# Kernel tuning notes

Hardware: AMD Instinct MI355X
Metric: run time of the kernel (lower is better)

## Reference

```python
import jax, jax.numpy as jnp
import numpy as np
import math

B, T, C, H, S = 2, 2048, 1024, 16, 16
HD = C // H
EPS = 1e-5


def setup_inputs() -> dict:
    key = jax.random.key(0)
    ks = jax.random.split(key, 20)
    sc = 1.0 / math.sqrt(C)
    inp = {
        "x": jax.random.normal(ks[0], (B, T, C), jnp.float32),
        # A_log_fwd: log(arange(1..S)) repeated over dim (as in __init__)
        "A_log": jnp.log(jnp.tile(jnp.arange(1, S + 1, dtype=jnp.float32), (C, 1))),
        # Linear weights stored (in, out); apply as x @ W + b
        "Wd": jax.random.normal(ks[1], (C, C), jnp.float32) * sc,
        "bd": jnp.full((C,), -3.0, jnp.float32),
        "WB": jax.random.normal(ks[2], (C, S), jnp.float32) * sc,
        "WC": jax.random.normal(ks[3], (C, S), jnp.float32) * sc,
        "Wq": jax.random.normal(ks[4], (C, C), jnp.float32) * sc,
        "bq": jnp.zeros((C,), jnp.float32),
        "Wk": jax.random.normal(ks[5], (C, C), jnp.float32) * sc,
        "bk": jnp.zeros((C,), jnp.float32),
        "Wv": jax.random.normal(ks[6], (C, C), jnp.float32) * sc,
        "bv": jnp.zeros((C,), jnp.float32),
        "Wx": jax.random.normal(ks[7], (C, C), jnp.float32) * sc,
        "bx": jnp.zeros((C,), jnp.float32),
        "Wo": jax.random.normal(ks[8], (C, C), jnp.float32) * sc,
        "bo": jnp.zeros((C,), jnp.float32),
        "ln_g": jnp.ones((C,), jnp.float32),
        "ln_b": jnp.zeros((C,), jnp.float32),
        "temp": jnp.full((1, H, 1, 1), 0.5, jnp.float32),
    }
    return inp


def _forward(x, A_log, Wd, bd, WB, WC, Wq, bq, Wk, bk, Wv, bv, Wx, bx, Wo, bo, ln_g, ln_b, temp):
    x_base = x @ Wx + bx                      # (B,T,C)
    delta = jax.nn.softplus(x @ Wd + bd)      # (B,T,C)
    B_mat = x @ WB                            # (B,T,S)
    C_mat = x @ WC                            # (B,T,S)
    A = -jnp.exp(A_log)                       # (C,S)

    def scan_fn(h, inp):
        xb_t, d_t, B_t, C_t = inp             # (B,C),(B,C),(B,S),(B,S)
        bar_A = jnp.exp(d_t[..., None] * A)   # (B,C,S)
        h = bar_A * h + (d_t * xb_t)[..., None] * B_t[:, None, :]
        y = jnp.einsum('bcs,bs->bc', h, C_t)
        return h, y

    h0 = jnp.zeros((B, C, S), x.dtype)
    xs = (jnp.swapaxes(x_base, 0, 1), jnp.swapaxes(delta, 0, 1),
          jnp.swapaxes(B_mat, 0, 1), jnp.swapaxes(C_mat, 0, 1))
    _, ys = jax.lax.scan(scan_fn, h0, xs)
    out_fwd = jnp.swapaxes(ys, 0, 1)          # (B,T,C)

    # LayerNorm(x_base + out_fwd)
    hyb = x_base + out_fwd
    mu = hyb.mean(-1, keepdims=True)
    var = hyb.var(-1, keepdims=True)
    hybrid = (hyb - mu) * jax.lax.rsqrt(var + EPS) * ln_g + ln_b

    def heads(W, b):
        return (hybrid @ W + b).reshape(B, T, H, HD).transpose(0, 2, 1, 3)

    Q, K, V = heads(Wq, bq), heads(Wk, bk), heads(Wv, bv)
    scores = jnp.einsum('bhqd,bhkd->bhqk', Q, K) / math.sqrt(HD)
    scores = scores * jax.nn.softplus(temp)
    mask = jnp.tril(jnp.ones((T, T), bool))
    scores = jnp.where(mask[None, None], scores, -jnp.inf)
    attn = jax.nn.softmax(scores, axis=-1)
    out = jnp.einsum('bhqk,bhkd->bhqd', attn, V).transpose(0, 2, 1, 3).reshape(B, T, C)
    return out @ Wo + bo


def reference(x, A_log, Wd, bd, WB, WC, Wq, bq, Wk, bk, Wv, bv, Wx, bx, Wo, bo, ln_g, ln_b, temp):
    return _forward(x, A_log, Wd, bd, WB, WC, Wq, bq, Wk, bk, Wv, bv, Wx, bx, Wo, bo, ln_g, ln_b, temp)
```

## Files before the change

### kernel.cpp

```cpp
#include <hip/hip_runtime.h>
#include <math.h>

#define B_  2
#define T_  2048
#define C_  1024
#define H_  16
#define S_  16
#define HD_ 64
#define NCH 32
#define CHL 64

typedef short  short8  __attribute__((ext_vector_type(8)));
typedef unsigned short ushort8 __attribute__((ext_vector_type(8)));
typedef unsigned short ushort4v __attribute__((ext_vector_type(4)));
typedef float  f32x4   __attribute__((ext_vector_type(4)));

__device__ __forceinline__ float softplus_f(float v) {
    return fmaxf(v, 0.f) + log1pf(__expf(-fabsf(v)));
}

__device__ __forceinline__ unsigned short f2bf(float x) {
    unsigned u = __float_as_uint(x);
    u += 0x7fffu + ((u >> 16) & 1u);
    return (unsigned short)(u >> 16);
}

__global__ __launch_bounds__(256) void cast_bf16(const float* __restrict__ in,
                                                 unsigned short* __restrict__ out,
                                                 int n4)
{
    int i = blockIdx.x * 256 + threadIdx.x;
    if (i >= n4) return;
    float4 v = ((const float4*)in)[i];
    ushort4v o = {f2bf(v.x), f2bf(v.y), f2bf(v.z), f2bf(v.w)};
    ((ushort4v*)out)[i] = o;
}

__device__ __forceinline__ void wtrans_body(const float* __restrict__ W,
                                            unsigned short* __restrict__ WT,
                                            int bx, int by, int tid)
{
    __shared__ float t[32][33];
    const int n0 = bx * 32, k0 = by * 32;
    const int tx = tid & 31, ty = tid >> 5;
#pragma unroll
    for (int p = 0; p < 4; ++p)
        t[ty + p * 8][tx] = W[(size_t)(k0 + ty + p * 8) * C_ + n0 + tx];
    __syncthreads();
#pragma unroll
    for (int p = 0; p < 4; ++p)
        WT[(size_t)(n0 + ty + p * 8) * C_ + k0 + tx] = f2bf(t[tx][ty + p * 8]);
}

__global__ __launch_bounds__(256) void wtrans(const float* __restrict__ W,
                                              unsigned short* __restrict__ WT)
{
    wtrans_body(W, WT, blockIdx.x, blockIdx.y, threadIdx.x);
}

__global__ __launch_bounds__(256) void wtrans_multi(
    const float* __restrict__ Wx, const float* __restrict__ Wd,
    const float* __restrict__ Wq, const float* __restrict__ Wk,
    const float* __restrict__ Wv,
    unsigned short* __restrict__ Astack, unsigned short* __restrict__ Wqkv)
{
    const float* src;
    unsigned short* dst;
    switch (blockIdx.z) {
        case 0: src = Wx; dst = Astack; break;
        case 1: src = Wd; dst = Astack + (size_t)1024 * 1024; break;
        case 2: src = Wq; dst = Wqkv; break;
        case 3: src = Wk; dst = Wqkv + (size_t)1024 * 1024; break;
        default: src = Wv; dst = Wqkv + (size_t)2048 * 1024; break;
    }
    wtrans_body(src, dst, blockIdx.x, blockIdx.y, threadIdx.x);
}

__global__ __launch_bounds__(256) void prep_misc(
    const float* __restrict__ WB, const float* __restrict__ WC,
    const float* __restrict__ bx, const float* __restrict__ bd,
    const float* __restrict__ bq, const float* __restrict__ bk,
    const float* __restrict__ bv,
    unsigned short* __restrict__ Astack, float* __restrict__ biasPD,
    float* __restrict__ biasQKV)
{
    int gid = blockIdx.x * 256 + threadIdx.x;
    if (gid < 32768) {
        int w = gid >> 14, rem = gid & 16383;
        int s = rem >> 10, k = rem & 1023;
        const float* src = w ? WC : WB;
        Astack[(size_t)(2048 + w * 16 + s) * 1024 + k] = f2bf(src[k * 16 + s]);
    } else {
        int id = gid - 32768;
        if (id < 2176) {
            biasPD[id] = id < 1024 ? bx[id] : (id < 2048 ? bd[id - 1024] : 0.f);
        } else {
            int id2 = id - 2176;
            if (id2 < 3072)
                biasQKV[id2] = id2 < 1024 ? bq[id2]
                             : (id2 < 2048 ? bk[id2 - 1024] : bv[id2 - 2048]);
        }
    }
}

__global__ __launch_bounds__(256) void gemm_mfma(
    const unsigned short* __restrict__ A, const unsigned short* __restrict__ Bm,
    const float* __restrict__ bias,
    void* __restrict__ outv, void* __restrict__ out2,
    void* __restrict__ out3, void* __restrict__ out4,
    int M, int N, int K, int lda, int mode)
{
    __shared__ __align__(16) unsigned short As[4096];
    __shared__ __align__(16) unsigned short Bs[4096];

    const int tid = threadIdx.x;
    const int w = tid >> 6, lane = tid & 63;
    const int lq = lane & 15, lg = lane >> 4;
    const int wm = w >> 1, wn = w & 1;
    const int mBase = blockIdx.y * 128, nBase = blockIdx.x * 128;

    A  += (size_t)blockIdx.z * K;
    Bm += (size_t)blockIdx.z * K;

    const int c0 = tid, c1 = tid + 256;
    const int rA0 = ((c0 >> 6) << 4) + (c0 & 15), kO0 = ((c0 >> 4) & 3) << 3;
    const int rA1 = ((c1 >> 6) << 4) + (c1 & 15), kO1 = ((c1 >> 4) & 3) << 3;

    f32x4 acc[4][4];
#pragma unroll
    for (int i = 0; i < 4; ++i)
#pragma unroll
        for (int j = 0; j < 4; ++j) acc[i][j] = (f32x4){0.f, 0.f, 0.f, 0.f};

    const unsigned short* ga0 = A  + (size_t)(mBase + rA0) * lda + kO0;
    const unsigned short* ga1 = A  + (size_t)(mBase + rA1) * lda + kO1;
    const unsigned short* gb0 = Bm + (size_t)(nBase + rA0) * lda + kO0;
    const unsigned short* gb1 = Bm + (size_t)(nBase + rA1) * lda + kO1;

    ushort8 pa0, pa1, pb0, pb1;
    #define PREF(k0v)                                      \
        do {                                               \
            pa0 = *(const ushort8*)(ga0 + (k0v));          \
            pa1 = *(const ushort8*)(ga1 + (k0v));          \
            pb0 = *(const ushort8*)(gb0 + (k0v));          \
            pb1 = *(const ushort8*)(gb1 + (k0v));          \
        } while (0)

    PREF(0);
    for (int k0 = 0; k0 < K; k0 += 32) {
        __syncthreads();
        *(ushort8*)&As[c0 * 8] = pa0;
        *(ushort8*)&As[c1 * 8] = pa1;
        *(ushort8*)&Bs[c0 * 8] = pb0;
        *(ushort8*)&Bs[c1 * 8] = pb1;
        __syncthreads();
        if (k0 + 32 < K) PREF(k0 + 32);
        short8 a[4], b[4];
#pragma unroll
        for (int i = 0; i < 4; ++i)
            a[i] = *(const short8*)&As[((wm * 4 + i) * 64 + lg * 16 + lq) * 8];
#pragma unroll
        for (int j = 0; j < 4; ++j)
            b[j] = *(const short8*)&Bs[((wn * 4 + j) * 64 + lg * 16 + lq) * 8];
#pragma unroll
        for (int i = 0; i < 4; ++i)
#pragma unroll
            for (int j = 0; j < 4; ++j)
                acc[i][j] = __builtin_amdgcn_mfma_f32_16x16x32_bf16(
                    a[i], b[j], acc[i][j], 0, 0, 0);
    }
    #undef PREF

    if (mode == 0) {
        float* O = blockIdx.z ? (float*)out2 : (float*)outv;
#pragma unroll
        for (int i = 0; i < 4; ++i) {
            int Rb = mBase + wm * 64 + i * 16 + lg * 4;
#pragma unroll
            for (int j = 0; j < 4; ++j) {
                int Cg = nBase + wn * 64 + j * 16 + lq;
#pragma unroll
                for (int r = 0; r < 4; ++r)
                    O[(size_t)(Rb + r) * N + Cg] = acc[i][j][r];
            }
        }
    } else if (mode == 1) {
        float* xbaseT = (float*)outv;
        float* deltaT = (float*)out2;
        float* BmT    = (float*)out3;
        float* CmT    = (float*)out4;
#pragma unroll
        for (int i = 0; i < 4; ++i) {
            int Rb = mBase + wm * 64 + i * 16 + lg * 4;
            if (Rb >= 2080) continue;
            float bb[4];
#pragma unroll
            for (int r = 0; r < 4; ++r) bb[r] = bias[Rb + r];
#pragma unroll
            for (int j = 0; j < 4; ++j) {
                int Cg = nBase + wn * 64 + j * 16 + lq;
                int b = Cg >> 11, t = Cg & (T_ - 1);
#pragma unroll
                for (int r = 0; r < 4; ++r) {
                    int R = Rb + r;
                    float v = acc[i][j][r] + bb[r];
                    if (Rb < 1024) {
                        xbaseT[((size_t)b * C_ + R) * T_ + t] = v;
                    } else if (Rb < 2048) {
                        deltaT[((size_t)b * C_ + (R - 1024)) * T_ + t] =
                            softplus_f(v);
                    } else if (Rb < 2064) {
                        BmT[((size_t)b * S_ + (R - 2048)) * T_ + t] = v;
                    } else {
                        CmT[((size_t)b * S_ + (R - 2064)) * T_ + t] = v;
                    }
                }
            }
        }
    } else {
        unsigned short* Qb  = (unsigned short*)outv;
        unsigned short* Kb  = (unsigned short*)out2;
        unsigned short* VTb = (unsigned short*)out3;
#pragma unroll
        for (int j = 0; j < 4; ++j) {
            int Cg = nBase + wn * 64 + j * 16 + lq;
            int reg = Cg >> 10, c = Cg & 1023;
            int h = c >> 6, hd = c & 63;
            float bb = bias[Cg];
#pragma unroll
            for (int i = 0; i < 4; ++i) {
                int Rb = mBase + wm * 64 + i * 16 + lg * 4;
#pragma unroll
                for (int r = 0; r < 4; ++r) {
                    int R = Rb + r, b = R >> 11, t = R & (T_ - 1);
                    unsigned short o = f2bf(acc[i][j][r] + bb);
                    if (reg == 0)
                        Qb[(((size_t)(b * H_ + h) * T_ + t) * HD_) + hd] = o;
                    else if (reg == 1)
                        Kb[(((size_t)(b * H_ + h) * T_ + t) * HD_) + hd] = o;
                    else
                        VTb[(((size_t)(b * H_ + h) * HD_ + hd) * T_) + t] = o;
                }
            }
        }
    }
}

__global__ __launch_bounds__(256) void combine_out(
    const float* __restrict__ p0, const float* __restrict__ p1,
    const float* __restrict__ bo, float* __restrict__ out)
{
    int i = blockIdx.x * 256 + threadIdx.x;
    float4 a = ((const float4*)p0)[i];
    float4 b = ((const float4*)p1)[i];
    float4 bb = ((const float4*)bo)[i & 255];
    float4 o = {a.x + b.x + bb.x, a.y + b.y + bb.y,
                a.z + b.z + bb.z, a.w + b.w + bb.w};
    ((float4*)out)[i] = o;
}

__global__ __launch_bounds__(256) void scan_partial(
    const float* __restrict__ xbaseT, const float* __restrict__ deltaT,
    const float* __restrict__ BmT, const float* __restrict__ A_log,
    float4* __restrict__ Pbuf, float4* __restrict__ Lbuf)
{
    const int tid = threadIdx.x;
    const int s4 = tid & 3;
    const int cm = tid >> 2;
    const int cg = blockIdx.x & 15;
    const int k  = (blockIdx.x >> 4) & (NCH - 1);
    const int b  = blockIdx.x >> 9;
    const int c  = cg * 64 + cm;

    float a[4];
#pragma unroll
    for (int j = 0; j < 4; ++j)
        a[j] = -__expf(A_log[c * S_ + s4 * 4 + j]);

    const int tb = k * CHL;
    const float* dp = deltaT + ((size_t)b * C_ + c) * T_ + tb;
    const float* xp = xbaseT + ((size_t)b * C_ + c) * T_ + tb;
    const float* bp = BmT + ((size_t)(b * S_ + s4 * 4)) * T_ + tb;

    float L[4] = {0.f, 0.f, 0.f, 0.f};
    float sumd = 0.f;
    for (int t0 = 0; t0 < CHL; t0 += 4) {
        float4 d4 = *(const float4*)&dp[t0];
        float4 x4 = *(const float4*)&xp[t0];
        float dv[4] = {d4.x, d4.y, d4.z, d4.w};
        float xv[4] = {x4.x, x4.y, x4.z, x4.w};
        float bv[4][4];
#pragma unroll
        for (int j = 0; j < 4; ++j) {
            float4 b4 = *(const float4*)&bp[(size_t)j * T_ + t0];
            bv[j][0] = b4.x; bv[j][1] = b4.y; bv[j][2] = b4.z; bv[j][3] = b4.w;
        }
#pragma unroll
        for (int q = 0; q < 4; ++q) {
            float u = dv[q] * xv[q];
            sumd += dv[q];
#pragma unroll
            for (int j = 0; j < 4; ++j)
                L[j] = fmaf(__expf(dv[q] * a[j]), L[j], u * bv[j][q]);
        }
    }
    int gid = blockIdx.x * 256 + tid;
    float4 P4 = {__expf(a[0] * sumd), __expf(a[1] * sumd),
                 __expf(a[2] * sumd), __expf(a[3] * sumd)};
    float4 L4 = {L[0], L[1], L[2], L[3]};
    Pbuf[gid] = P4;
    Lbuf[gid] = L4;
}

__global__ __launch_bounds__(256) void scan_final(
    const float* __restrict__ xbaseT, const float* __restrict__ deltaT,
    const float* __restrict__ BmT, const float* __restrict__ CmT,
    const float* __restrict__ A_log, const float4* __restrict__ Pbuf,
    const float4* __restrict__ Lbuf, float* __restrict__ hyb)
{
    const int tid = threadIdx.x;
    const int s4 = tid & 3;
    const int cm = tid >> 2;
    const int cg = blockIdx.x & 15;
    const int k  = (blockIdx.x >> 4) & (NCH - 1);
    const int b  = blockIdx.x >> 9;
    const int c  = cg * 64 + cm;

    float h[4] = {0.f, 0.f, 0.f, 0.f};
    for (int k2 = 0; k2 < k; ++k2) {
        int gid2 = (((b * NCH + k2) << 4) + cg) * 256 + tid;
        float4 P4 = Pbuf[gid2];
        float4 L4 = Lbuf[gid2];
        h[0] = fmaf(P4.x, h[0], L4.x);
        h[1] = fmaf(P4.y, h[1], L4.y);
        h[2] = fmaf(P4.z, h[2], L4.z);
        h[3] = fmaf(P4.w, h[3], L4.w);
    }

    float a[4];
#pragma unroll
    for (int j = 0; j < 4; ++j)
        a[j] = -__expf(A_log[c * S_ + s4 * 4 + j]);

    const int tb = k * CHL;
    const float* dp = deltaT + ((size_t)b * C_ + c) * T_ + tb;
    const float* xp = xbaseT + ((size_t)b * C_ + c) * T_ + tb;
    const float* bp = BmT + ((size_t)(b * S_ + s4 * 4)) * T_ + tb;
    const float* cp = CmT + ((size_t)(b * S_ + s4 * 4)) * T_ + tb;
    float* hp = hyb + ((size_t)b * T_ + tb) * C_ + c;

    for (int t0 = 0; t0 < CHL; t0 += 4) {
        float4 d4 = *(const float4*)&dp[t0];
        float4 x4 = *(const float4*)&xp[t0];
        float dv[4] = {d4.x, d4.y, d4.z, d4.w};
        float xv[4] = {x4.x, x4.y, x4.z, x4.w};
        float bv[4][4], cv[4][4];
#pragma unroll
        for (int j = 0; j < 4; ++j) {
            float4 b4 = *(const float4*)&bp[(size_t)j * T_ + t0];
            float4 c4 = *(const float4*)&cp[(size_t)j * T_ + t0];
            bv[j][0] = b4.x; bv[j][1] = b4.y; bv[j][2] = b4.z; bv[j][3] = b4.w;
            cv[j][0] = c4.x; cv[j][1] = c4.y; cv[j][2] = c4.z; cv[j][3] = c4.w;
        }
#pragma unroll
        for (int q = 0; q < 4; ++q) {
            float u = dv[q] * xv[q];
#pragma unroll
            for (int j = 0; j < 4; ++j)
                h[j] = fmaf(__expf(dv[q] * a[j]), h[j], u * bv[j][q]);
            float y = h[0] * cv[0][q];
            y = fmaf(h[1], cv[1][q], y);
            y = fmaf(h[2], cv[2][q], y);
            y = fmaf(h[3], cv[3][q], y);
            y += __shfl_xor(y, 1, 64);
            y += __shfl_xor(y, 2, 64);
            if (s4 == 0) hp[(size_t)(t0 + q) * C_] = xv[q] + y;
        }
    }
}

__global__ __launch_bounds__(256) void layernorm_kernel(
    const float* __restrict__ in, const float* __restrict__ g,
    const float* __restrict__ beta, unsigned short* __restrict__ out)
{
    const int row = blockIdx.x;
    const float* rp = in + (size_t)row * C_;
    const int c = threadIdx.x * 4;
    float4 v = *(const float4*)&rp[c];
    float sum = v.x + v.y + v.z + v.w;
    float sq = v.x * v.x + v.y * v.y + v.z * v.z + v.w * v.w;
#pragma unroll
    for (int off = 1; off < 64; off <<= 1) {
        sum += __shfl_xor(sum, off, 64);
        sq += __shfl_xor(sq, off, 64);
    }
    __shared__ float sS[4], sQ[4];
    int wave = threadIdx.x >> 6, lane = threadIdx.x & 63;
    if (lane == 0) { sS[wave] = sum; sQ[wave] = sq; }
    __syncthreads();
    sum = sS[0] + sS[1] + sS[2] + sS[3];
    sq = sQ[0] + sQ[1] + sQ[2] + sQ[3];
    const float mu = sum * (1.f / C_);
    const float var = sq * (1.f / C_) - mu * mu;
    const float rstd = rsqrtf(var + 1e-5f);
    float4 gg = *(const float4*)&g[c];
    float4 bb = *(const float4*)&beta[c];
    ushort4v o;
    o.x = f2bf((v.x - mu) * rstd * gg.x + bb.x);
    o.y = f2bf((v.y - mu) * rstd * gg.y + bb.y);
    o.z = f2bf((v.z - mu) * rstd * gg.z + bb.z);
    o.w = f2bf((v.w - mu) * rstd * gg.w + bb.w);
    *(ushort4v*)&out[(size_t)row * C_ + c] = o;
}

#define BKT 128
#define KP  72
#define VP  136
__global__ __launch_bounds__(256) void attn_mfma(
    const unsigned short* __restrict__ Q, const unsigned short* __restrict__ K,
    const unsigned short* __restrict__ VT, const float* __restrict__ temp,
    unsigned short* __restrict__ out)
{
    __shared__ __align__(16) unsigned short Ks[BKT * KP];
    __shared__ __align__(16) unsigned short Vs[80 * VP];
    __shared__ __align__(16) unsigned short Ps[64 * VP];

    const int tid = threadIdx.x;
    const int w = tid >> 6, lane = tid & 63;
    const int lq = lane & 15, lg = lane >> 4;
    const int p  = blockIdx.x & 15;
    const int bh = blockIdx.x >> 4;
    const int b = bh >> 4, h = bh & 15;

    const float scale = softplus_f(temp[h]) * 0.125f;
    const unsigned short* Qp = Q + (size_t)bh * T_ * HD_;
    const unsigned short* Kp = K + (size_t)bh * T_ * HD_;
    const unsigned short* Vp = VT + (size_t)bh * HD_ * T_;

    {
        int r = 64 + (tid >> 4), o = (tid & 15) * 8;
        ushort8 ones = {0x3f80, 0x3f80, 0x3f80, 0x3f80,
                        0x3f80, 0x3f80, 0x3f80, 0x3f80};
        *(ushort8*)&Vs[r * VP + o] = ones;
    }

    ushort8 kreg[4], vreg[4];
    #define LOADKV(jtv)                                                        \
        do {                                                                   \
            int kb = (jtv) * BKT;                                              \
            _Pragma("unroll")                                                  \
            for (int q2 = 0; q2 < 4; ++q2) {                                   \
                int c = tid + q2 * 256;                                        \
                kreg[q2] = *(const ushort8*)&Kp[(size_t)(kb + (c >> 3)) * HD_  \
                                                + (c & 7) * 8];                \
                vreg[q2] = *(const ushort8*)&Vp[(size_t)(c >> 4) * T_ + kb     \
                                                + (c & 15) * 8];               \
            }                                                                  \
        } while (0)

    for (int half = 0; half < 2; ++half) {
        const int qi = half ? p : (31 - p);
        const int qbase = qi * 64;
        const int nT = (qbase + 64 + BKT - 1) / BKT;

        short8 qf[2];
#pragma unroll
        for (int s = 0; s < 2; ++s)
            qf[s] = *(const short8*)&Qp[(size_t)(qbase + w * 16 + lq) * HD_
                                        + s * 32 + lg * 8];
        LOADKV(0);

        float m_i[4];
        f32x4 o[5];
#pragma unroll
        for (int r = 0; r < 4; ++r) m_i[r] = -INFINITY;
#pragma unroll
        for (int j = 0; j < 5; ++j) o[j] = (f32x4){0.f, 0.f, 0.f, 0.f};

        for (int jt = 0; jt < nT; ++jt) {
            const int kbase = jt * BKT;
            const bool last = (jt == nT - 1);
            __syncthreads();
#pragma unroll
            for (int q2 = 0; q2 < 4; ++q2) {
                int c = tid + q2 * 256;
                *(ushort8*)&Ks[(c >> 3) * KP + (c & 7) * 8] = kreg[q2];
                *(ushort8*)&Vs[(c >> 4) * VP + (c & 15) * 8] = vreg[q2];
            }
            __syncthreads();
            if (jt + 1 < nT) LOADKV(jt + 1);

            f32x4 sacc[8];
#pragma unroll
            for (int j = 0; j < 8; ++j) sacc[j] = (f32x4){0.f, 0.f, 0.f, 0.f};
#pragma unroll
            for (int s = 0; s < 2; ++s) {
#pragma unroll
                for (int j = 0; j < 8; ++j) {
                    short8 kf = *(const short8*)&Ks[(j * 16 + lq) * KP
                                                    + s * 32 + lg * 8];
                    sacc[j] = __builtin_amdgcn_mfma_f32_16x16x32_bf16(
                        qf[s], kf, sacc[j], 0, 0, 0);
                }
            }

#pragma unroll
            for (int r = 0; r < 4; ++r) {
                int qrow = qbase + w * 16 + lg * 4 + r;
                float sv[8];
#pragma unroll
                for (int j = 0; j < 8; ++j) {
                    sv[j] = sacc[j][r] * scale;
                    if (last && (kbase + j * 16 + lq > qrow)) sv[j] = -INFINITY;
                }
                float mx = sv[0];
#pragma unroll
                for (int j = 1; j < 8; ++j) mx = fmaxf(mx, sv[j]);
                mx = fmaxf(mx, __shfl_xor(mx, 1, 64));
                mx = fmaxf(mx, __shfl_xor(mx, 2, 64));
                mx = fmaxf(mx, __shfl_xor(mx, 4, 64));
                mx = fmaxf(mx, __shfl_xor(mx, 8, 64));
                float mnew = fmaxf(m_i[r], mx);
                float alpha = __expf(m_i[r] - mnew);
                m_i[r] = mnew;
#pragma unroll
                for (int j = 0; j < 5; ++j) o[j][r] *= alpha;
#pragma unroll
                for (int j = 0; j < 8; ++j)
                    Ps[(w * 16 + lg * 4 + r) * VP + j * 16 + lq] =
                        f2bf(__expf(sv[j] - mnew));
            }

#pragma unroll
            for (int s2 = 0; s2 < 4; ++s2) {
                short8 pf = *(const short8*)&Ps[(w * 16 + lq) * VP
                                                + s2 * 32 + lg * 8];
#pragma unroll
                for (int j = 0; j < 5; ++j) {
                    short8 vf = *(const short8*)&Vs[(j * 16 + lq) * VP
                                                    + s2 * 32 + lg * 8];
                    o[j] = __builtin_amdgcn_mfma_f32_16x16x32_bf16(
                        pf, vf, o[j], 0, 0, 0);
                }
            }
        }

#pragma unroll
        for (int r = 0; r < 4; ++r) {
            float inv = 1.f / o[4][r];
            int qrow = qbase + w * 16 + lg * 4 + r;
#pragma unroll
            for (int j = 0; j < 4; ++j)
                out[((size_t)(b * T_ + qrow)) * C_ + h * 64 + j * 16 + lq] =
                    f2bf(o[j][r] * inv);
        }
    }
    #undef LOADKV
}

extern "C" void kernel_launch(void* const* d_in, const int* in_sizes, int n_in,
                              void* d_out, int out_size, void* d_ws, size_t ws_size,
                              hipStream_t stream)
{
    const float* x     = (const float*)d_in[0];
    const float* A_log = (const float*)d_in[1];
    const float* Wd    = (const float*)d_in[2];
    const float* bd    = (const float*)d_in[3];
    const float* WB    = (const float*)d_in[4];
    const float* WC    = (const float*)d_in[5];
    const float* Wq    = (const float*)d_in[6];
    const float* bq    = (const float*)d_in[7];
    const float* Wk    = (const float*)d_in[8];
    const float* bk    = (const float*)d_in[9];
    const float* Wv    = (const float*)d_in[10];
    const float* bv    = (const float*)d_in[11];
    const float* Wx    = (const float*)d_in[12];
    const float* bx    = (const float*)d_in[13];
    const float* Wo    = (const float*)d_in[14];
    const float* bo    = (const float*)d_in[15];
    const float* ln_g  = (const float*)d_in[16];
    const float* ln_b  = (const float*)d_in[17];
    const float* temp  = (const float*)d_in[18];

    char* wsb = (char*)d_ws;
    const size_t MB = 1024 * 1024;
    const size_t HMB = 512 * 1024;
    unsigned short* xb      = (unsigned short*)(wsb);
    float4* Pbuf            = (float4*)(wsb);
    float4* Lbuf            = (float4*)(wsb + 4 * MB);
    unsigned short* hybrid  = (unsigned short*)(wsb);
    float* P1               = (float*)(wsb);
    unsigned short* Astack  = (unsigned short*)(wsb + 8 * MB);
    float* biasPD           = (float*)(wsb + 8 * MB + (size_t)2176 * 2048);
    float* biasQKV          = biasPD + 2176;
    unsigned short* WqkvT   = (unsigned short*)(wsb + 12 * MB + HMB);
    unsigned short* WoT     = (unsigned short*)(wsb + 18 * MB + HMB);
    float* deltaT           = (float*)(wsb + 18 * MB + HMB);
    float* xbaseT           = (float*)(wsb + 34 * MB + HMB);
    float* hyb              = (float*)(wsb + 50 * MB + HMB);
    float* BmT              = (float*)(wsb + 66 * MB + HMB);
    float* CmT              = BmT + (size_t)B_ * S_ * T_;
    unsigned short* Qb      = (unsigned short*)(wsb + 20 * MB + HMB);
    unsigned short* Kb      = (unsigned short*)(wsb + 28 * MB + HMB);
    unsigned short* VTb     = (unsigned short*)(wsb + 36 * MB + HMB);
    unsigned short* attnO   = (unsigned short*)(wsb + 44 * MB + HMB);
    float* P0               = (float*)(wsb + 20 * MB + HMB);

    cast_bf16<<<4096, 256, 0, stream>>>(x, xb, (B_ * T_ * C_) / 4);
    wtrans_multi<<<dim3(32, 32, 5), 256, 0, stream>>>(Wx, Wd, Wq, Wk, Wv,
                                                      Astack, WqkvT);
    prep_misc<<<149, 256, 0, stream>>>(WB, WC, bx, bd, bq, bk, bv,
                                       Astack, biasPD, biasQKV);

    gemm_mfma<<<dim3(32, 17, 1), 256, 0, stream>>>(
        Astack, xb, biasPD, xbaseT, deltaT, BmT, CmT,
        2176, 4096, 1024, 1024, 1);

    const int scanBlocks = B_ * NCH * (C_ / 64);
    scan_partial<<<scanBlocks, 256, 0, stream>>>(xbaseT, deltaT, BmT, A_log,
                                                 Pbuf, Lbuf);
    scan_final<<<scanBlocks, 256, 0, stream>>>(xbaseT, deltaT, BmT, CmT, A_log,
                                               Pbuf, Lbuf, hyb);

    layernorm_kernel<<<B_ * T_, 256, 0, stream>>>(hyb, ln_g, ln_b, hybrid);

    gemm_mfma<<<dim3(24, 32, 1), 256, 0, stream>>>(
        hybrid, WqkvT, biasQKV, Qb, Kb, VTb, nullptr,
        4096, 3072, 1024, 1024, 2);

    attn_mfma<<<B_ * H_ * 16, 256, 0, stream>>>(Qb, Kb, VTb, temp, attnO);

    wtrans<<<dim3(32, 32), 256, 0, stream>>>(Wo, WoT);
    gemm_mfma<<<dim3(8, 32, 2), 256, 0, stream>>>(
        attnO, WoT, nullptr, P0, P1, nullptr, nullptr,
        4096, 1024, 512, 1024, 0);
    combine_out<<<4096, 256, 0, stream>>>(P0, P1, bo, (float*)d_out);
}
```

Baseline: 474.7 us.

## Double-buffer GEMM shared-memory tiles with two-stage register prefetch

Replaces the single-buffered LDS tile loop in the MFMA GEMM with two LDS buffers and two sets of prefetch registers. Each iteration stores the next tile into the alternate buffer while computing on the current one. This removes one of the two barriers per k-step and overlaps global loads further ahead. The cost is doubled LDS use (32KB per block) and more registers, which may reduce occupancy. The hand-written waitcnt/barrier asm could also be fragile if stores are reordered.

```diff
diff --git a/kernel.cpp b/kernel.cpp
--- a/kernel.cpp
+++ b/kernel.cpp
@@ -110,8 +110,8 @@
     void* __restrict__ out3, void* __restrict__ out4,
     int M, int N, int K, int lda, int mode)
 {
-    __shared__ __align__(16) unsigned short As[4096];
-    __shared__ __align__(16) unsigned short Bs[4096];
+    __shared__ __align__(16) unsigned short As[2][4096];
+    __shared__ __align__(16) unsigned short Bs[2][4096];
 
     const int tid = threadIdx.x;
     const int w = tid >> 6, lane = tid & 63;
@@ -137,39 +137,61 @@
     const unsigned short* gb0 = Bm + (size_t)(nBase + rA0) * lda + kO0;
     const unsigned short* gb1 = Bm + (size_t)(nBase + rA1) * lda + kO1;
 
-    ushort8 pa0, pa1, pb0, pb1;
-    #define PREF(k0v)                                      \
+    ushort8 pA0, pA1, pB0, pB1;
+    ushort8 qA0, qA1, qB0, qB1;
+
+    #define PREFS(SA0, SA1, SB0, SB1, k0v)                 \
         do {                                               \
-            pa0 = *(const ushort8*)(ga0 + (k0v));          \
-            pa1 = *(const ushort8*)(ga1 + (k0v));          \
-            pb0 = *(const ushort8*)(gb0 + (k0v));          \
-            pb1 = *(const ushort8*)(gb1 + (k0v));          \
+            SA0 = *(const ushort8*)(ga0 + (k0v));          \
+            SA1 = *(const ushort8*)(ga1 + (k0v));          \
+            SB0 = *(const ushort8*)(gb0 + (k0v));          \
+            SB1 = *(const ushort8*)(gb1 + (k0v));          \
         } while (0)
-
-    PREF(0);
-    for (int k0 = 0; k0 < K; k0 += 32) {
-        __syncthreads();
-        *(ushort8*)&As[c0 * 8] = pa0;
-        *(ushort8*)&As[c1 * 8] = pa1;
-        *(ushort8*)&Bs[c0 * 8] = pb0;
-        *(ushort8*)&Bs[c1 * 8] = pb1;
-        __syncthreads();
-        if (k0 + 32 < K) PREF(k0 + 32);
-        short8 a[4], b[4];
-#pragma unroll
-        for (int i = 0; i < 4; ++i)
-            a[i] = *(const short8*)&As[((wm * 4 + i) * 64 + lg * 16 + lq) * 8];
-#pragma unroll
-        for (int j = 0; j < 4; ++j)
-            b[j] = *(const short8*)&Bs[((wn * 4 + j) * 64 + lg * 16 + lq) * 8];
-#pragma unroll
-        for (int i = 0; i < 4; ++i)
-#pragma unroll
-            for (int j = 0; j < 4; ++j)
-                acc[i][j] = __builtin_amdgcn_mfma_f32_16x16x32_bf16(
-                    a[i], b[j], acc[i][j], 0, 0, 0);
-    }
-    #undef PREF
+    #define STORES(SA0, SA1, SB0, SB1, bufv)               \
+        do {                                               \
+            *(ushort8*)&As[bufv][c0 * 8] = SA0;            \
+            *(ushort8*)&As[bufv][c1 * 8] = SA1;            \
+            *(ushort8*)&Bs[bufv][c0 * 8] = SB0;            \
+            *(ushort8*)&Bs[bufv][c1 * 8] = SB1;            \
+        } while (0)
+    #define LBAR() asm volatile("s_waitcnt lgkmcnt(0)\n\ts_barrier" ::: "memory")
+    #define COMPUTE(bufv)                                                       \
+        do {                                                                    \
+            short8 a[4], b[4];                                                  \
+            _Pragma("unroll")                                                   \
+            for (int i = 0; i < 4; ++i)                                         \
+                a[i] = *(const short8*)&As[bufv][((wm * 4 + i) * 64 + lg * 16 + lq) * 8]; \
+            _Pragma("unroll")                                                   \
+            for (int j = 0; j < 4; ++j)                                         \
+                b[j] = *(const short8*)&Bs[bufv][((wn * 4 + j) * 64 + lg * 16 + lq) * 8]; \
+            _Pragma("unroll")                                                   \
+            for (int i = 0; i < 4; ++i)                                         \
+                _Pragma("unroll")                                               \
+                for (int j = 0; j < 4; ++j)                                     \
+                    acc[i][j] = __builtin_amdgcn_mfma_f32_16x16x32_bf16(        \
+                        a[i], b[j], acc[i][j], 0, 0, 0);                        \
+        } while (0)
+
+    PREFS(pA0, pA1, pB0, pB1, 0);
+    STORES(pA0, pA1, pB0, pB1, 0);
+    PREFS(pA0, pA1, pB0, pB1, 32);
+    PREFS(qA0, qA1, qB0, qB1, 64);
+    LBAR();
+
+    for (int k0 = 0; k0 < K; k0 += 64) {
+        if (k0 + 32 < K) STORES(pA0, pA1, pB0, pB1, 1);
+        if (k0 + 96 < K) PREFS(pA0, pA1, pB0, pB1, k0 + 96);
+        COMPUTE(0);
+        LBAR();
+        if (k0 + 64 < K) STORES(qA0, qA1, qB0, qB1, 0);
+        if (k0 + 128 < K) PREFS(qA0, qA1, qB0, qB1, k0 + 128);
+        if (k0 + 32 < K) COMPUTE(1);
+        LBAR();
+    }
+    #undef PREFS
+    #undef STORES
+    #undef LBAR
+    #undef COMPUTE
 
     if (mode == 0) {
         float* O = blockIdx.z ? (float*)out2 : (float*)outv;
```

Measured after the change: 474.0 us. About the same (-0.1%).

## Store xbase and delta as bf16 for the scan and merge prep kernels

Applied to the files above, without the earlier changes.

The projection GEMM now writes the transposed x_base and delta intermediates as bf16 instead of fp32. Both scan kernels load them as 8-wide bf16 vectors and widen them to float, processing 8 timesteps per iteration. This halves the memory traffic of these large intermediates, at some cost in accuracy in the recurrence and in the residual x_base added to the scan output. The bf16 cast of x, the weight transposes and the misc prep are also fused into a single launch to save two kernel launches.

```diff
diff --git a/kernel.cpp b/kernel.cpp
--- a/kernel.cpp
+++ b/kernel.cpp
@@ -25,15 +25,8 @@
     return (unsigned short)(u >> 16);
 }
 
-__global__ __launch_bounds__(256) void cast_bf16(const float* __restrict__ in,
-                                                 unsigned short* __restrict__ out,
-                                                 int n4)
-{
-    int i = blockIdx.x * 256 + threadIdx.x;
-    if (i >= n4) return;
-    float4 v = ((const float4*)in)[i];
-    ushort4v o = {f2bf(v.x), f2bf(v.y), f2bf(v.z), f2bf(v.w)};
-    ((ushort4v*)out)[i] = o;
+__device__ __forceinline__ float bf2f(unsigned short u) {
+    return __uint_as_float((unsigned)u << 16);
 }
 
 __device__ __forceinline__ void wtrans_body(const float* __restrict__ W,
@@ -58,47 +51,58 @@
     wtrans_body(W, WT, blockIdx.x, blockIdx.y, threadIdx.x);
 }
 
-__global__ __launch_bounds__(256) void wtrans_multi(
+__global__ __launch_bounds__(256) void prep_all(
+    const float* __restrict__ x,
     const float* __restrict__ Wx, const float* __restrict__ Wd,
     const float* __restrict__ Wq, const float* __restrict__ Wk,
     const float* __restrict__ Wv,
-    unsigned short* __restrict__ Astack, unsigned short* __restrict__ Wqkv)
-{
-    const float* src;
-    unsigned short* dst;
-    switch (blockIdx.z) {
-        case 0: src = Wx; dst = Astack; break;
-        case 1: src = Wd; dst = Astack + (size_t)1024 * 1024; break;
-        case 2: src = Wq; dst = Wqkv; break;
-        case 3: src = Wk; dst = Wqkv + (size_t)1024 * 1024; break;
-        default: src = Wv; dst = Wqkv + (size_t)2048 * 1024; break;
-    }
-    wtrans_body(src, dst, blockIdx.x, blockIdx.y, threadIdx.x);
-}
-
-__global__ __launch_bounds__(256) void prep_misc(
     const float* __restrict__ WB, const float* __restrict__ WC,
     const float* __restrict__ bx, const float* __restrict__ bd,
     const float* __restrict__ bq, const float* __restrict__ bk,
     const float* __restrict__ bv,
-    unsigned short* __restrict__ Astack, float* __restrict__ biasPD,
+    unsigned short* __restrict__ xb, unsigned short* __restrict__ Astack,
+    unsigned short* __restrict__ Wqkv, float* __restrict__ biasPD,
     float* __restrict__ biasQKV)
 {
-    int gid = blockIdx.x * 256 + threadIdx.x;
-    if (gid < 32768) {
-        int w = gid >> 14, rem = gid & 16383;
-        int s = rem >> 10, k = rem & 1023;
-        const float* src = w ? WC : WB;
-        Astack[(size_t)(2048 + w * 16 + s) * 1024 + k] = f2bf(src[k * 16 + s]);
+    const int blk = blockIdx.x;
+    const int tid = threadIdx.x;
+    if (blk < 4096) {
+        int i = blk * 256 + tid;
+        float4 v = ((const float4*)x)[i];
+        ushort4v o = {f2bf(v.x), f2bf(v.y), f2bf(v.z), f2bf(v.w)};
+        ((ushort4v*)xb)[i] = o;
+    } else if (blk < 9216) {
+        int z = (blk - 4096) >> 10, rem = (blk - 4096) & 1023;
+        const float* src;
+        unsigned short* dst;
+        switch (z) {
+            case 0: src = Wx; dst = Astack; break;
+            case 1: src = Wd; dst = Astack + (size_t)1024 * 1024; break;
+            case 2: src = Wq; dst = Wqkv; break;
+            case 3: src = Wk; dst = Wqkv + (size_t)1024 * 1024; break;
+            default: src = Wv; dst = Wqkv + (size_t)2048 * 1024; break;
+        }
+        wtrans_body(src, dst, rem & 31, rem >> 5, tid);
     } else {
-        int id = gid - 32768;
-        if (id < 2176) {
-            biasPD[id] = id < 1024 ? bx[id] : (id < 2048 ? bd[id - 1024] : 0.f);
+        int gid = (blk - 9216) * 256 + tid;
+        if (gid < 32768) {
+            int w = gid >> 14, rem = gid & 16383;
+            int s = rem >> 10, k = rem & 1023;
+            const float* src = w ? WC : WB;
+            Astack[(size_t)(2048 + w * 16 + s) * 1024 + k] =
+                f2bf(src[k * 16 + s]);
         } else {
-            int id2 = id - 2176;
-            if (id2 < 3072)
-                biasQKV[id2] = id2 < 1024 ? bq[id2]
-                             : (id2 < 2048 ? bk[id2 - 1024] : bv[id2 - 2048]);
+            int id = gid - 32768;
+            if (id < 2176) {
+                biasPD[id] = id < 1024 ? bx[id]
+                           : (id < 2048 ? bd[id - 1024] : 0.f);
+            } else {
+                int id2 = id - 2176;
+                if (id2 < 3072)
+                    biasQKV[id2] = id2 < 1024 ? bq[id2]
+                                 : (id2 < 2048 ? bk[id2 - 1024]
+                                               : bv[id2 - 2048]);
+            }
         }
     }
 }
@@ -185,10 +189,10 @@
             }
         }
     } else if (mode == 1) {
-        float* xbaseT = (float*)outv;
-        float* deltaT = (float*)out2;
-        float* BmT    = (float*)out3;
-        float* CmT    = (float*)out4;
+        unsigned short* xbaseT = (unsigned short*)outv;
+        unsigned short* deltaT = (unsigned short*)out2;
+        float* BmT = (float*)out3;
+        float* CmT = (float*)out4;
 #pragma unroll
         for (int i = 0; i < 4; ++i) {
             int Rb = mBase + wm * 64 + i * 16 + lg * 4;
@@ -205,10 +209,10 @@
                     int R = Rb + r;
                     float v = acc[i][j][r] + bb[r];
                     if (Rb < 1024) {
-                        xbaseT[((size_t)b * C_ + R) * T_ + t] = v;
+                        xbaseT[((size_t)b * C_ + R) * T_ + t] = f2bf(v);
                     } else if (Rb < 2048) {
                         deltaT[((size_t)b * C_ + (R - 1024)) * T_ + t] =
-                            softplus_f(v);
+                            f2bf(softplus_f(v));
                     } else if (Rb < 2064) {
                         BmT[((size_t)b * S_ + (R - 2048)) * T_ + t] = v;
                     } else {
@@ -260,7 +264,8 @@
 }
 
 __global__ __launch_bounds__(256) void scan_partial(
-    const float* __restrict__ xbaseT, const float* __restrict__ deltaT,
+    const unsigned short* __restrict__ xbaseT,
+    const unsigned short* __restrict__ deltaT,
     const float* __restrict__ BmT, const float* __restrict__ A_log,
     float4* __restrict__ Pbuf, float4* __restrict__ Lbuf)
 {
@@ -278,25 +283,28 @@
         a[j] = -__expf(A_log[c * S_ + s4 * 4 + j]);
 
     const int tb = k * CHL;
-    const float* dp = deltaT + ((size_t)b * C_ + c) * T_ + tb;
-    const float* xp = xbaseT + ((size_t)b * C_ + c) * T_ + tb;
+    const unsigned short* dp = deltaT + ((size_t)b * C_ + c) * T_ + tb;
+    const unsigned short* xp = xbaseT + ((size_t)b * C_ + c) * T_ + tb;
     const float* bp = BmT + ((size_t)(b * S_ + s4 * 4)) * T_ + tb;
 
     float L[4] = {0.f, 0.f, 0.f, 0.f};
     float sumd = 0.f;
-    for (int t0 = 0; t0 < CHL; t0 += 4) {
-        float4 d4 = *(const float4*)&dp[t0];
-        float4 x4 = *(const float4*)&xp[t0];
-        float dv[4] = {d4.x, d4.y, d4.z, d4.w};
-        float xv[4] = {x4.x, x4.y, x4.z, x4.w};
-        float bv[4][4];
+    for (int t0 = 0; t0 < CHL; t0 += 8) {
+        ushort8 d8 = *(const ushort8*)&dp[t0];
+        ushort8 x8 = *(const ushort8*)&xp[t0];
+        float dv[8], xv[8];
+#pragma unroll
+        for (int e = 0; e < 8; ++e) { dv[e] = bf2f(d8[e]); xv[e] = bf2f(x8[e]); }
+        float bv[4][8];
 #pragma unroll
         for (int j = 0; j < 4; ++j) {
-            float4 b4 = *(const float4*)&bp[(size_t)j * T_ + t0];
-            bv[j][0] = b4.x; bv[j][1] = b4.y; bv[j][2] = b4.z; bv[j][3] = b4.w;
-        }
-#pragma unroll
-        for (int q = 0; q < 4; ++q) {
+            float4 b4a = *(const float4*)&bp[(size_t)j * T_ + t0];
+            float4 b4b = *(const float4*)&bp[(size_t)j * T_ + t0 + 4];
+            bv[j][0] = b4a.x; bv[j][1] = b4a.y; bv[j][2] = b4a.z; bv[j][3] = b4a.w;
+            bv[j][4] = b4b.x; bv[j][5] = b4b.y; bv[j][6] = b4b.z; bv[j][7] = b4b.w;
+        }
+#pragma unroll
+        for (int q = 0; q < 8; ++q) {
             float u = dv[q] * xv[q];
             sumd += dv[q];
 #pragma unroll
@@ -313,7 +321,8 @@
 }
 
 __global__ __launch_bounds__(256) void scan_final(
-    const float* __restrict__ xbaseT, const float* __restrict__ deltaT,
+    const unsigned short* __restrict__ xbaseT,
+    const unsigned short* __restrict__ deltaT,
     const float* __restrict__ BmT, const float* __restrict__ CmT,
     const float* __restrict__ A_log, const float4* __restrict__ Pbuf,
     const float4* __restrict__ Lbuf, float* __restrict__ hyb)
@@ -343,27 +352,32 @@
         a[j] = -__expf(A_log[c * S_ + s4 * 4 + j]);
 
     const int tb = k * CHL;
-    const float* dp = deltaT + ((size_t)b * C_ + c) * T_ + tb;
-    const float* xp = xbaseT + ((size_t)b * C_ + c) * T_ + tb;
+    const unsigned short* dp = deltaT + ((size_t)b * C_ + c) * T_ + tb;
+    const unsigned short* xp = xbaseT + ((size_t)b * C_ + c) * T_ + tb;
     const float* bp = BmT + ((size_t)(b * S_ + s4 * 4)) * T_ + tb;
     const float* cp = CmT + ((size_t)(b * S_ + s4 * 4)) * T_ + tb;
     float* hp = hyb + ((size_t)b * T_ + tb) * C_ + c;
 
-    for (int t0 = 0; t0 < CHL; t0 += 4) {
-        float4 d4 = *(const float4*)&dp[t0];
-        float4 x4 = *(const float4*)&xp[t0];
-        float dv[4] = {d4.x, d4.y, d4.z, d4.w};
-        float xv[4] = {x4.x, x4.y, x4.z, x4.w};
-        float bv[4][4], cv[4][4];
+    for (int t0 = 0; t0 < CHL; t0 += 8) {
+        ushort8 d8 = *(const ushort8*)&dp[t0];
+        ushort8 x8 = *(const ushort8*)&xp[t0];
+        float dv[8], xv[8];
+#pragma unroll
+        for (int e = 0; e < 8; ++e) { dv[e] = bf2f(d8[e]); xv[e] = bf2f(x8[e]); }
+        float bv[4][8], cv[4][8];
 #pragma unroll
         for (int j = 0; j < 4; ++j) {
-            float4 b4 = *(const float4*)&bp[(size_t)j * T_ + t0];
-            float4 c4 = *(const float4*)&cp[(size_t)j * T_ + t0];
-            bv[j][0] = b4.x; bv[j][1] = b4.y; bv[j][2] = b4.z; bv[j][3] = b4.w;
-            cv[j][0] = c4.x; cv[j][1] = c4.y; cv[j][2] = c4.z; cv[j][3] = c4.w;
-        }
-#pragma unroll
-        for (int q = 0; q < 4; ++q) {
+            float4 b4a = *(const float4*)&bp[(size_t)j * T_ + t0];
+            float4 b4b = *(const float4*)&bp[(size_t)j * T_ + t0 + 4];
+            float4 c4a = *(const float4*)&cp[(size_t)j * T_ + t0];
+            float4 c4b = *(const float4*)&cp[(size_t)j * T_ + t0 + 4];
+            bv[j][0] = b4a.x; bv[j][1] = b4a.y; bv[j][2] = b4a.z; bv[j][3] = b4a.w;
+            bv[j][4] = b4b.x; bv[j][5] = b4b.y; bv[j][6] = b4b.z; bv[j][7] = b4b.w;
+            cv[j][0] = c4a.x; cv[j][1] = c4a.y; cv[j][2] = c4a.z; cv[j][3] = c4a.w;
+            cv[j][4] = c4b.x; cv[j][5] = c4b.y; cv[j][6] = c4b.z; cv[j][7] = c4b.w;
+        }
+#pragma unroll
+        for (int q = 0; q < 8; ++q) {
             float u = dv[q] * xv[q];
 #pragma unroll
             for (int j = 0; j < 4; ++j)
@@ -595,8 +609,8 @@
     float* biasQKV          = biasPD + 2176;
     unsigned short* WqkvT   = (unsigned short*)(wsb + 12 * MB + HMB);
     unsigned short* WoT     = (unsigned short*)(wsb + 18 * MB + HMB);
-    float* deltaT           = (float*)(wsb + 18 * MB + HMB);
-    float* xbaseT           = (float*)(wsb + 34 * MB + HMB);
+    unsigned short* deltaT  = (unsigned short*)(wsb + 18 * MB + HMB);
+    unsigned short* xbaseT  = (unsigned short*)(wsb + 34 * MB + HMB);
     float* hyb              = (float*)(wsb + 50 * MB + HMB);
     float* BmT              = (float*)(wsb + 66 * MB + HMB);
     float* CmT              = BmT + (size_t)B_ * S_ * T_;
@@ -606,11 +620,9 @@
     unsigned short* attnO   = (unsigned short*)(wsb + 44 * MB + HMB);
     float* P0               = (float*)(wsb + 20 * MB + HMB);
 
-    cast_bf16<<<4096, 256, 0, stream>>>(x, xb, (B_ * T_ * C_) / 4);
-    wtrans_multi<<<dim3(32, 32, 5), 256, 0, stream>>>(Wx, Wd, Wq, Wk, Wv,
-                                                      Astack, WqkvT);
-    prep_misc<<<149, 256, 0, stream>>>(WB, WC, bx, bd, bq, bk, bv,
-                                       Astack, biasPD, biasQKV);
+    prep_all<<<9365, 256, 0, stream>>>(x, Wx, Wd, Wq, Wk, Wv, WB, WC,
+                                       bx, bd, bq, bk, bv,
+                                       xb, Astack, WqkvT, biasPD, biasQKV);
 
     gemm_mfma<<<dim3(32, 17, 1), 256, 0, stream>>>(
         Astack, xb, biasPD, xbaseT, deltaT, BmT, CmT,
```

Result: no change. 481.3 us (+1.4%).
